# Kernel optimization log

Measured on AMD Instinct MI355X. Metric: run time of the kernel, lower is better.

Reference implementation:

```python
import jax, jax.numpy as jnp
import numpy as np

N = 100000   # nodes
E = 800000   # edges (avg degree 8)
D = 128      # input_dim == output_dim
H = 4        # num_heads
DH = D // H  # head_dim = 32


def setup_inputs() -> dict:
    key = jax.random.key(0)
    ks = jax.random.split(key, 12)
    s = 1.0 / np.sqrt(D)
    x = jax.random.normal(ks[0], (N, D), jnp.float32)
    row = jnp.sort(jax.random.randint(ks[1], (E,), 0, N))  # destination (query) nodes
    col = jax.random.randint(ks[2], (E,), 0, N)            # source (key/value) nodes
    Wq = jax.random.normal(ks[3], (D, D), jnp.float32) * s
    bq = jax.random.normal(ks[4], (D,), jnp.float32) * 0.01
    Wk = jax.random.normal(ks[5], (D, D), jnp.float32) * s
    bk = jax.random.normal(ks[6], (D,), jnp.float32) * 0.01
    Wv = jax.random.normal(ks[7], (D, D), jnp.float32) * s
    bv = jax.random.normal(ks[8], (D,), jnp.float32) * 0.01
    Wo = jax.random.normal(ks[9], (D, D), jnp.float32) * s
    bo = jax.random.normal(ks[10], (D,), jnp.float32) * 0.01
    return {"x": x, "row": row, "col": col, "Wq": Wq, "bq": bq, "Wk": Wk,
            "bk": bk, "Wv": Wv, "bv": bv, "Wo": Wo, "bo": bo}


def reference(x, row, col, Wq, bq, Wk, bk, Wv, bv, Wo, bo):
    n = x.shape[0]
    # projections; reshape (N, head_dim, num_heads) exactly as the torch code
    # NOTE: source scales q by k.size(-1)**0.5 == sqrt(num_heads) (quirk, kept faithful)
    scale = jnp.asarray(H, x.dtype) ** 0.5
    q = ((x @ Wq.T + bq).reshape(n, DH, H)) / scale
    k = (x @ Wk.T + bk).reshape(n, DH, H)
    v = (x @ Wv.T + bv).reshape(n, DH, H)
    # bsddmm: per-edge, per-head scores s[e,h] = q[row[e],:,h] . k[col[e],:,h]
    s = jnp.einsum('edh,edh->eh', q[row], k[col])  # (E, H)
    # sparse row-wise softmax over incoming edges of each destination node
    m = jax.ops.segment_max(s, row, num_segments=n)      # (N, H)
    e = jnp.exp(s - m[row])                               # (E, H)
    z = jax.ops.segment_sum(e, row, num_segments=n)      # (N, H)
    a = e / z[row]                                        # (E, H) attention weights
    # bspmm: y[i,:,h] = sum_{e: row[e]=i} a[e,h] * v[col[e],:,h]
    y = jax.ops.segment_sum(a[:, None, :] * v[col], row, num_segments=n)  # (N, DH, H)
    return y.reshape(n, D) @ Wo.T + bo
```

## Files before the change

### kernel.cpp

```cpp
#include <hip/hip_runtime.h>
#include <hip/hip_bf16.h>
#include <hip/hip_fp16.h>
#include <math.h>

#define D 128
#define H 4

typedef __attribute__((ext_vector_type(8))) short bf16x8;
typedef __attribute__((ext_vector_type(4))) float f32x4;

__device__ __forceinline__ unsigned short f32_to_bf16_rne(float f) {
    union { float f; unsigned u; } c; c.f = f;
    unsigned u = c.u;
    return (unsigned short)((u + 0x7FFFu + ((u >> 16) & 1u)) >> 16);
}
__device__ __forceinline__ float bf16_to_f32(unsigned short h) {
    union { unsigned u; float f; } c; c.u = ((unsigned)h) << 16;
    return c.f;
}

__global__ __launch_bounds__(256) void convert_w(
    const float* __restrict__ Wq, const float* __restrict__ Wk,
    const float* __restrict__ Wv, const float* __restrict__ Wo,
    unsigned short* __restrict__ wh, unsigned short* __restrict__ wl)
{
    int i = blockIdx.x * blockDim.x + threadIdx.x;
    if (i >= D * D) return;
    int r = i >> 7;
    int c = i & 127;
    int pr = ((r & 3) << 5) | (r >> 2);
    int pc = ((c & 3) << 5) | (c >> 2);
    const float* Ws[4] = {Wq, Wk, Wv, Wo};
#pragma unroll
    for (int m = 0; m < 4; ++m) {
        float f = Ws[m][i];
        unsigned short h = f32_to_bf16_rne(f);
        unsigned short l = f32_to_bf16_rne(f - bf16_to_f32(h));
        int dst = (m < 3) ? (pr * D + c) : (r * D + pc);
        wh[m * D * D + dst] = h;
        wl[m * D * D + dst] = l;
    }
}

#define RT 64

template<int NSEL>
__global__ __launch_bounds__(512) void gemm_fused(
    const float* __restrict__ A,
    const unsigned short* __restrict__ whAll, const unsigned short* __restrict__ wlAll,
    const float* __restrict__ b0, const float* __restrict__ b1,
    const float* __restrict__ b2,
    void* __restrict__ o0, void* __restrict__ o1, void* __restrict__ o2,
    float scale0, int n, int wbase, int halfmask, int permBias)
{
    __shared__ unsigned short Ah[RT * 128];
    __shared__ unsigned short Al[RT * 128];

    const int wid  = threadIdx.x >> 6;
    const int lane = threadIdx.x & 63;
    const int quad = lane >> 4;
    const int l16  = lane & 15;
    const int m0   = blockIdx.x * RT;

    for (int idx = threadIdx.x; idx < RT * 16; idx += 512) {
        int r  = idx >> 4;
        int c8 = idx & 15;
        int rg = m0 + r; if (rg > n - 1) rg = n - 1;
        const float4* src = (const float4*)(A + (size_t)rg * D + c8 * 8);
        float4 f0 = src[0], f1 = src[1];
        float fa[8] = {f0.x, f0.y, f0.z, f0.w, f1.x, f1.y, f1.z, f1.w};
        union { bf16x8 v; unsigned short s[8]; } hv, lv;
#pragma unroll
        for (int j = 0; j < 8; ++j) {
            unsigned short hh = f32_to_bf16_rne(fa[j]);
            hv.s[j] = hh;
            lv.s[j] = f32_to_bf16_rne(fa[j] - bf16_to_f32(hh));
        }
        int cs = ((c8 ^ (r & 15)) * 8);
        *(bf16x8*)&Ah[r * 128 + cs] = hv.v;
        *(bf16x8*)&Al[r * 128 + cs] = lv.v;
    }
    __syncthreads();

#pragma unroll 1
    for (int sel = 0; sel < NSEL; ++sel) {
        const unsigned short* wh = whAll + (size_t)(wbase + sel) * D * D;
        const unsigned short* wl = wlAll + (size_t)(wbase + sel) * D * D;
        const float* bias = (sel == 0) ? b0 : (sel == 1 ? b1 : b2);
        void* out        = (sel == 0) ? o0 : (sel == 1 ? o1 : o2);
        const float scale = (sel == 0) ? scale0 : 1.0f;
        const bool halfOut = (halfmask >> sel) & 1;

        const unsigned short* wrh = wh + (size_t)(wid * 16 + l16) * D + quad * 8;
        const unsigned short* wrl = wl + (size_t)(wid * 16 + l16) * D + quad * 8;
        bf16x8 bh[4], bl[4];
#pragma unroll
        for (int kc = 0; kc < 4; ++kc) {
            bh[kc] = *(const bf16x8*)(wrh + kc * 32);
            bl[kc] = *(const bf16x8*)(wrl + kc * 32);
        }

        f32x4 acc[4];
#pragma unroll
        for (int rt = 0; rt < 4; ++rt) acc[rt] = (f32x4){0.f, 0.f, 0.f, 0.f};

#pragma unroll
        for (int kc = 0; kc < 4; ++kc) {
            const int cs = ((quad + 4 * kc) ^ l16) * 8;
            bf16x8 ah[4], al[4];
#pragma unroll
            for (int rt = 0; rt < 4; ++rt) {
                const int r = rt * 16 + l16;
                ah[rt] = *(const bf16x8*)&Ah[r * 128 + cs];
                al[rt] = *(const bf16x8*)&Al[r * 128 + cs];
            }
#pragma unroll
            for (int rt = 0; rt < 4; ++rt)
                acc[rt] = __builtin_amdgcn_mfma_f32_16x16x32_bf16(ah[rt], bh[kc], acc[rt], 0, 0, 0);
#pragma unroll
            for (int rt = 0; rt < 4; ++rt)
                acc[rt] = __builtin_amdgcn_mfma_f32_16x16x32_bf16(al[rt], bh[kc], acc[rt], 0, 0, 0);
#pragma unroll
            for (int rt = 0; rt < 4; ++rt)
                acc[rt] = __builtin_amdgcn_mfma_f32_16x16x32_bf16(ah[rt], bl[kc], acc[rt], 0, 0, 0);
        }

        const int colg = wid * 16 + l16;
        const int bidx = permBias ? (((colg & 31) << 2) | (colg >> 5)) : colg;
        const float bv = bias[bidx];
        if (halfOut) {
            __half* oph = (__half*)out;
#pragma unroll
            for (int rt = 0; rt < 4; ++rt) {
#pragma unroll
                for (int r = 0; r < 4; ++r) {
                    int rowg = m0 + rt * 16 + quad * 4 + r;
                    if (rowg < n)
                        oph[(size_t)rowg * D + colg] = __float2half(acc[rt][r] + bv);
                }
            }
        } else {
            float* opf = (float*)out;
#pragma unroll
            for (int rt = 0; rt < 4; ++rt) {
#pragma unroll
                for (int r = 0; r < 4; ++r) {
                    int rowg = m0 + rt * 16 + quad * 4 + r;
                    if (rowg < n)
                        opf[(size_t)rowg * D + colg] = (acc[rt][r] + bv) * scale;
                }
            }
        }
    }
}

__global__ void build_row_start(const int* __restrict__ row,
                                int* __restrict__ row_start, int n, int e)
{
    int i = blockIdx.x * blockDim.x + threadIdx.x;
    if (i > n) return;
    int lo = 0, hi = e;
    while (lo < hi) {
        int mid = (lo + hi) >> 1;
        if (row[mid] < i) lo = mid + 1; else hi = mid;
    }
    row_start[i] = lo;
}

#define MAXDEG 64
#define WPB 4

template<bool BIG>
__device__ __forceinline__ void edge_loop(
    int lane, int sub, int grp, int deg, int e0,
    const int* cmrow, const int* __restrict__ col,
    const float4 qa, const float4 qb,
    const __half* __restrict__ k, const __half* __restrict__ v,
    float& acc0, float& acc1, float& z)
{
    for (int e = 0; e < deg; e += 4) {
        const int ei = e + grp;
        int c0, c1, c2, c3, cs;
        if (!BIG) {
            const int4 cc = *(const int4*)&cmrow[e];
            c0 = cc.x; c1 = cc.y; c2 = cc.z; c3 = cc.w;
            cs = cmrow[ei < deg ? ei : deg - 1];
        } else {
            int es = ei < deg ? ei : deg - 1;
            cs = col[e0 + es];
            int e1 = e + 1 < deg ? e + 1 : deg - 1;
            int e2 = e + 2 < deg ? e + 2 : deg - 1;
            int e3 = e + 3 < deg ? e + 3 : deg - 1;
            c0 = col[e0 + e];
            c1 = col[e0 + e1];
            c2 = col[e0 + e2];
            c3 = col[e0 + e3];
        }
        __half2 v0 = ((const __half2*)(v + ((size_t)c0 << 7)))[lane];
        __half2 v1 = ((const __half2*)(v + ((size_t)c1 << 7)))[lane];
        __half2 v2 = ((const __half2*)(v + ((size_t)c2 << 7)))[lane];
        __half2 v3 = ((const __half2*)(v + ((size_t)c3 << 7)))[lane];
        union { bf16x8 v8; __half hx[8]; } ku;
        ku.v8 = *(const bf16x8*)(k + ((size_t)cs << 7) + sub * 8);
        float p = qa.x * __half2float(ku.hx[0]) + qa.y * __half2float(ku.hx[1])
                + qa.z * __half2float(ku.hx[2]) + qa.w * __half2float(ku.hx[3])
                + qb.x * __half2float(ku.hx[4]) + qb.y * __half2float(ku.hx[5])
                + qb.z * __half2float(ku.hx[6]) + qb.w * __half2float(ku.hx[7]);
        p += __shfl_xor(p, 1);
        p += __shfl_xor(p, 2);
        float ep = (ei < deg) ? __expf(p) : 0.f;
        float a0 = __shfl(ep,      4 * grp);
        float a1 = __shfl(ep, 16 + 4 * grp);
        float a2 = __shfl(ep, 32 + 4 * grp);
        float a3 = __shfl(ep, 48 + 4 * grp);
        z += (a0 + a1) + (a2 + a3);
        acc0 += a0 * __half2float(v0.x) + a1 * __half2float(v1.x)
              + a2 * __half2float(v2.x) + a3 * __half2float(v3.x);
        acc1 += a0 * __half2float(v0.y) + a1 * __half2float(v1.y)
              + a2 * __half2float(v2.y) + a3 * __half2float(v3.y);
    }
}

__global__ __launch_bounds__(WPB * 64) void edge_attn(
    const int* __restrict__ row_start,
    const float* __restrict__ q, const __half* __restrict__ k,
    const __half* __restrict__ v, const int* __restrict__ col,
    float* __restrict__ y, int n)
{
    __shared__ int cm[WPB][MAXDEG];

    const int wid  = threadIdx.x >> 6;
    const int lane = threadIdx.x & 63;
    const int node = blockIdx.x * WPB + wid;
    if (node >= n) return;

    const int e0  = row_start[node];
    const int deg = row_start[node + 1] - e0;
    const int sub = lane & 15;
    const int grp = lane >> 4;

    const float4* q4 = (const float4*)(q + (size_t)node * D) + sub * 2;
    const float4 qa = q4[0], qb = q4[1];

    float acc0 = 0.f, acc1 = 0.f, z = 0.f;

    if (deg <= MAXDEG) {
        const int dl4 = (deg + 3) & ~3;
        for (int i = lane; i < dl4; i += 64) {
            int ii = i < deg ? i : deg - 1;
            cm[wid][i] = col[e0 + ii];
        }
        edge_loop<false>(lane, sub, grp, deg, e0, cm[wid], col, qa, qb, k, v,
                         acc0, acc1, z);
    } else {
        edge_loop<true>(lane, sub, grp, deg, e0, cm[wid], col, qa, qb, k, v,
                        acc0, acc1, z);
    }

    const float rz = (z > 0.f) ? 1.f / z : 0.f;
    acc0 *= rz;
    acc1 *= rz;

    float2 o; o.x = acc0; o.y = acc1;
    ((float2*)y)[(size_t)node * 64 + lane] = o;
}

extern "C" void kernel_launch(void* const* d_in, const int* in_sizes, int n_in,
                              void* d_out, int out_size, void* d_ws, size_t ws_size,
                              hipStream_t stream)
{
    const float* x   = (const float*)d_in[0];
    const int*   row = (const int*)  d_in[1];
    const int*   col = (const int*)  d_in[2];
    const float* Wq  = (const float*)d_in[3];
    const float* bq  = (const float*)d_in[4];
    const float* Wk  = (const float*)d_in[5];
    const float* bk  = (const float*)d_in[6];
    const float* Wv  = (const float*)d_in[7];
    const float* bv  = (const float*)d_in[8];
    const float* Wo  = (const float*)d_in[9];
    const float* bo  = (const float*)d_in[10];
    float* out = (float*)d_out;

    const int n = in_sizes[0] / D;
    const int e = in_sizes[1];
    const size_t ND = (size_t)n * D;

    float* ws = (float*)d_ws;
    float*  q  = ws;
    __half* kh = (__half*)(ws + ND);
    __half* vh = kh + ND;
    float*  y  = ws + 2 * ND;
    unsigned short* wh = (unsigned short*)(ws + 3 * ND);
    unsigned short* wl = wh + 4 * D * D;
    int* row_start = (int*)(wl + 4 * D * D);

    const int gx = (n + RT - 1) / RT;

    convert_w<<<(D * D + 255) / 256, 256, 0, stream>>>(Wq, Wk, Wv, Wo, wh, wl);

    gemm_fused<3><<<gx, 512, 0, stream>>>(
        x, wh, wl, bq, bk, bv,
        (void*)q, (void*)kh, (void*)vh, 0.5f, n, 0, 6, 1);

    build_row_start<<<(n + 1 + 255) / 256, 256, 0, stream>>>(row, row_start, n, e);

    edge_attn<<<(n + WPB - 1) / WPB, WPB * 64, 0, stream>>>(
        row_start, q, kh, vh, col, y, n);

    gemm_fused<1><<<gx, 512, 0, stream>>>(
        y, wh, wl, bo, bo, bo,
        (void*)out, (void*)out, (void*)out, 1.0f, n, 3, 0, 0);
}
```

Measured before the change: 308.1 us.

## Make projection GEMMs persistent with double-buffered A tiles and per-block weight selection

The fused projection GEMM becomes a persistent kernel with a fixed grid. Each block is assigned one weight matrix, keeps its hi/lo weight fragments in registers, and loops over row tiles. It prefetches the next tile's activations into registers and splits them into a second LDS buffer while the current tile is computed. This aims to hide global-load latency and stop reloading weights per tile. The cost is that each activation tile is now read and split three times (once per Q/K/V block) instead of once, and LDS use doubles, which may reduce occupancy.

Result: faster. 272.8 us (-11.5%).

```diff
diff --git a/kernel.cpp b/kernel.cpp
--- a/kernel.cpp
+++ b/kernel.cpp
@@ -17,6 +17,21 @@
 __device__ __forceinline__ float bf16_to_f32(unsigned short h) {
     union { unsigned u; float f; } c; c.u = ((unsigned)h) << 16;
     return c.f;
+}
+
+__device__ __forceinline__ void split_store(const float4 f0, const float4 f1,
+                                            unsigned short* dh, unsigned short* dl)
+{
+    float fa[8] = {f0.x, f0.y, f0.z, f0.w, f1.x, f1.y, f1.z, f1.w};
+    union { bf16x8 v; unsigned short s[8]; } hv, lv;
+#pragma unroll
+    for (int j = 0; j < 8; ++j) {
+        unsigned short hh = f32_to_bf16_rne(fa[j]);
+        hv.s[j] = hh;
+        lv.s[j] = f32_to_bf16_rne(fa[j] - bf16_to_f32(hh));
+    }
+    *(bf16x8*)dh = hv.v;
+    *(bf16x8*)dl = lv.v;
 }
 
 __global__ __launch_bounds__(256) void convert_w(
@@ -44,60 +59,73 @@
 
 #define RT 64
 
-template<int NSEL>
-__global__ __launch_bounds__(512) void gemm_fused(
+__global__ __launch_bounds__(512) void gemm_pipe(
     const float* __restrict__ A,
     const unsigned short* __restrict__ whAll, const unsigned short* __restrict__ wlAll,
     const float* __restrict__ b0, const float* __restrict__ b1,
     const float* __restrict__ b2,
     void* __restrict__ o0, void* __restrict__ o1, void* __restrict__ o2,
-    float scale0, int n, int wbase, int halfmask, int permBias)
-{
-    __shared__ unsigned short Ah[RT * 128];
-    __shared__ unsigned short Al[RT * 128];
+    float scale0, int n, int wbase, int halfmask, int permBias,
+    int nsel, int gx)
+{
+    __shared__ unsigned short Ah[2][RT * 128];
+    __shared__ unsigned short Al[2][RT * 128];
+
+    const int sel    = blockIdx.x % nsel;
+    const int tile0  = blockIdx.x / nsel;
+    const int tstride = gridDim.x / nsel;
+
+    const unsigned short* wh = whAll + (size_t)(wbase + sel) * D * D;
+    const unsigned short* wl = wlAll + (size_t)(wbase + sel) * D * D;
+    const float* bias = (sel == 0) ? b0 : (sel == 1 ? b1 : b2);
+    void* out        = (sel == 0) ? o0 : (sel == 1 ? o1 : o2);
+    const float scale = (sel == 0) ? scale0 : 1.0f;
+    const bool halfOut = (halfmask >> sel) & 1;
 
     const int wid  = threadIdx.x >> 6;
     const int lane = threadIdx.x & 63;
     const int quad = lane >> 4;
     const int l16  = lane & 15;
-    const int m0   = blockIdx.x * RT;
-
-    for (int idx = threadIdx.x; idx < RT * 16; idx += 512) {
-        int r  = idx >> 4;
-        int c8 = idx & 15;
-        int rg = m0 + r; if (rg > n - 1) rg = n - 1;
-        const float4* src = (const float4*)(A + (size_t)rg * D + c8 * 8);
-        float4 f0 = src[0], f1 = src[1];
-        float fa[8] = {f0.x, f0.y, f0.z, f0.w, f1.x, f1.y, f1.z, f1.w};
-        union { bf16x8 v; unsigned short s[8]; } hv, lv;
-#pragma unroll
-        for (int j = 0; j < 8; ++j) {
-            unsigned short hh = f32_to_bf16_rne(fa[j]);
-            hv.s[j] = hh;
-            lv.s[j] = f32_to_bf16_rne(fa[j] - bf16_to_f32(hh));
-        }
-        int cs = ((c8 ^ (r & 15)) * 8);
-        *(bf16x8*)&Ah[r * 128 + cs] = hv.v;
-        *(bf16x8*)&Al[r * 128 + cs] = lv.v;
+
+    const unsigned short* wrh = wh + (size_t)(wid * 16 + l16) * D + quad * 8;
+    const unsigned short* wrl = wl + (size_t)(wid * 16 + l16) * D + quad * 8;
+    bf16x8 bh[4], bl[4];
+#pragma unroll
+    for (int kc = 0; kc < 4; ++kc) {
+        bh[kc] = *(const bf16x8*)(wrh + kc * 32);
+        bl[kc] = *(const bf16x8*)(wrl + kc * 32);
+    }
+
+    const int idxA = threadIdx.x;
+    const int idxB = threadIdx.x + 512;
+    const int rA = idxA >> 4, cA = idxA & 15;
+    const int rB = idxB >> 4, cB = idxB & 15;
+    const int dA = rA * 128 + ((cA ^ (rA & 15)) * 8);
+    const int dB = rB * 128 + ((cB ^ (rB & 15)) * 8);
+
+    {
+        int rgA = tile0 * RT + rA; if (rgA > n - 1) rgA = n - 1;
+        int rgB = tile0 * RT + rB; if (rgB > n - 1) rgB = n - 1;
+        const float4* pA = (const float4*)(A + (size_t)rgA * D + cA * 8);
+        const float4* pB = (const float4*)(A + (size_t)rgB * D + cB * 8);
+        float4 a0 = pA[0], a1 = pA[1], a2 = pB[0], a3 = pB[1];
+        split_store(a0, a1, &Ah[0][dA], &Al[0][dA]);
+        split_store(a2, a3, &Ah[0][dB], &Al[0][dB]);
     }
     __syncthreads();
 
-#pragma unroll 1
-    for (int sel = 0; sel < NSEL; ++sel) {
-        const unsigned short* wh = whAll + (size_t)(wbase + sel) * D * D;
-        const unsigned short* wl = wlAll + (size_t)(wbase + sel) * D * D;
-        const float* bias = (sel == 0) ? b0 : (sel == 1 ? b1 : b2);
-        void* out        = (sel == 0) ? o0 : (sel == 1 ? o1 : o2);
-        const float scale = (sel == 0) ? scale0 : 1.0f;
-        const bool halfOut = (halfmask >> sel) & 1;
-
-        const unsigned short* wrh = wh + (size_t)(wid * 16 + l16) * D + quad * 8;
-        const unsigned short* wrl = wl + (size_t)(wid * 16 + l16) * D + quad * 8;
-        bf16x8 bh[4], bl[4];
-#pragma unroll
-        for (int kc = 0; kc < 4; ++kc) {
-            bh[kc] = *(const bf16x8*)(wrh + kc * 32);
-            bl[kc] = *(const bf16x8*)(wrl + kc * 32);
+    int cur = 0;
+    for (int t = tile0; t < gx; t += tstride) {
+        const int tn = t + tstride;
+        const bool more = (tn < gx);
+
+        float4 a0, a1, a2, a3;
+        if (more) {
+            int rgA = tn * RT + rA; if (rgA > n - 1) rgA = n - 1;
+            int rgB = tn * RT + rB; if (rgB > n - 1) rgB = n - 1;
+            const float4* pA = (const float4*)(A + (size_t)rgA * D + cA * 8);
+            const float4* pB = (const float4*)(A + (size_t)rgB * D + cB * 8);
+            a0 = pA[0]; a1 = pA[1]; a2 = pB[0]; a3 = pB[1];
         }
 
         f32x4 acc[4];
@@ -111,8 +139,8 @@
 #pragma unroll
             for (int rt = 0; rt < 4; ++rt) {
                 const int r = rt * 16 + l16;
-                ah[rt] = *(const bf16x8*)&Ah[r * 128 + cs];
-                al[rt] = *(const bf16x8*)&Al[r * 128 + cs];
+                ah[rt] = *(const bf16x8*)&Ah[cur][r * 128 + cs];
+                al[rt] = *(const bf16x8*)&Al[cur][r * 128 + cs];
             }
 #pragma unroll
             for (int rt = 0; rt < 4; ++rt)
@@ -125,6 +153,7 @@
                 acc[rt] = __builtin_amdgcn_mfma_f32_16x16x32_bf16(ah[rt], bl[kc], acc[rt], 0, 0, 0);
         }
 
+        const int m0 = t * RT;
         const int colg = wid * 16 + l16;
         const int bidx = permBias ? (((colg & 31) << 2) | (colg >> 5)) : colg;
         const float bv = bias[bidx];
@@ -151,6 +180,13 @@
                 }
             }
         }
+
+        if (more) {
+            split_store(a0, a1, &Ah[cur ^ 1][dA], &Al[cur ^ 1][dA]);
+            split_store(a2, a3, &Ah[cur ^ 1][dB], &Al[cur ^ 1][dB]);
+        }
+        __syncthreads();
+        cur ^= 1;
     }
 }
 
@@ -299,16 +335,18 @@
 
     convert_w<<<(D * D + 255) / 256, 256, 0, stream>>>(Wq, Wk, Wv, Wo, wh, wl);
 
-    gemm_fused<3><<<gx, 512, 0, stream>>>(
+    gemm_pipe<<<768, 512, 0, stream>>>(
         x, wh, wl, bq, bk, bv,
-        (void*)q, (void*)kh, (void*)vh, 0.5f, n, 0, 6, 1);
+        (void*)q, (void*)kh, (void*)vh, 0.5f, n, 0, 6, 1,
+        3, gx);
 
     build_row_start<<<(n + 1 + 255) / 256, 256, 0, stream>>>(row, row_start, n, e);
 
     edge_attn<<<(n + WPB - 1) / WPB, WPB * 64, 0, stream>>>(
         row_start, q, kh, vh, col, y, n);
 
-    gemm_fused<1><<<gx, 512, 0, stream>>>(
+    gemm_pipe<<<512, 512, 0, stream>>>(
         y, wh, wl, bo, bo, bo,
-        (void*)out, (void*)out, (void*)out, 1.0f, n, 3, 0, 0);
-}
+        (void*)out, (void*)out, (void*)out, 1.0f, n, 3, 0, 0,
+        1, gx);
+}
```

## Replace LDS-staged GEMM with direct-register 16-row tiles split across projections

Applied to the files above, without the earlier changes.

Replaces the shared-memory staged 64-row GEMM with a kernel in which each block handles 16 rows, loads and splits the fp32 input into bf16 hi/lo pairs directly in registers, and has each wave compute 32 output columns. The three Q/K/V projections become separate grid-y blocks instead of a serial loop inside one block. This removes the LDS staging and the barrier and raises parallelism. In exchange, each input row is now read and converted three times, once per projection, and the weight fragments are reloaded by many more, smaller blocks.

After: 462.2 us. 50.0% more time.

```diff
diff --git a/kernel.cpp b/kernel.cpp
--- a/kernel.cpp
+++ b/kernel.cpp
@@ -42,10 +42,8 @@
     }
 }
 
-#define RT 64
-
-template<int NSEL>
-__global__ __launch_bounds__(512) void gemm_fused(
+
+__global__ __launch_bounds__(256) void gemm_direct(
     const float* __restrict__ A,
     const unsigned short* __restrict__ whAll, const unsigned short* __restrict__ wlAll,
     const float* __restrict__ b0, const float* __restrict__ b1,
@@ -53,102 +51,79 @@
     void* __restrict__ o0, void* __restrict__ o1, void* __restrict__ o2,
     float scale0, int n, int wbase, int halfmask, int permBias)
 {
-    __shared__ unsigned short Ah[RT * 128];
-    __shared__ unsigned short Al[RT * 128];
+    const int sel = blockIdx.y;
+    const unsigned short* wh = whAll + (size_t)(wbase + sel) * D * D;
+    const unsigned short* wl = wlAll + (size_t)(wbase + sel) * D * D;
+    const float* bias = (sel == 0) ? b0 : (sel == 1 ? b1 : b2);
+    void* out        = (sel == 0) ? o0 : (sel == 1 ? o1 : o2);
+    const float scale = (sel == 0) ? scale0 : 1.0f;
+    const bool halfOut = (halfmask >> sel) & 1;
 
     const int wid  = threadIdx.x >> 6;
     const int lane = threadIdx.x & 63;
     const int quad = lane >> 4;
     const int l16  = lane & 15;
-    const int m0   = blockIdx.x * RT;
-
-    for (int idx = threadIdx.x; idx < RT * 16; idx += 512) {
-        int r  = idx >> 4;
-        int c8 = idx & 15;
-        int rg = m0 + r; if (rg > n - 1) rg = n - 1;
-        const float4* src = (const float4*)(A + (size_t)rg * D + c8 * 8);
-        float4 f0 = src[0], f1 = src[1];
+    const int m0   = blockIdx.x * 16;
+
+    bf16x8 bh[2][4], bl[2][4];
+#pragma unroll
+    for (int s = 0; s < 2; ++s) {
+        const unsigned short* wrh = wh + (size_t)(wid * 32 + s * 16 + l16) * D + quad * 8;
+        const unsigned short* wrl = wl + (size_t)(wid * 32 + s * 16 + l16) * D + quad * 8;
+#pragma unroll
+        for (int kc = 0; kc < 4; ++kc) {
+            bh[s][kc] = *(const bf16x8*)(wrh + kc * 32);
+            bl[s][kc] = *(const bf16x8*)(wrl + kc * 32);
+        }
+    }
+
+    int rga = m0 + l16; if (rga > n - 1) rga = n - 1;
+    const float* ap = A + (size_t)rga * D + quad * 8;
+
+    f32x4 acc0 = (f32x4){0.f, 0.f, 0.f, 0.f};
+    f32x4 acc1 = (f32x4){0.f, 0.f, 0.f, 0.f};
+
+#pragma unroll
+    for (int kc = 0; kc < 4; ++kc) {
+        const float4 f0 = *(const float4*)(ap + kc * 32);
+        const float4 f1 = *(const float4*)(ap + kc * 32 + 4);
         float fa[8] = {f0.x, f0.y, f0.z, f0.w, f1.x, f1.y, f1.z, f1.w};
-        union { bf16x8 v; unsigned short s[8]; } hv, lv;
+        union { bf16x8 v; unsigned short s[8]; } ah, al;
 #pragma unroll
         for (int j = 0; j < 8; ++j) {
             unsigned short hh = f32_to_bf16_rne(fa[j]);
-            hv.s[j] = hh;
-            lv.s[j] = f32_to_bf16_rne(fa[j] - bf16_to_f32(hh));
-        }
-        int cs = ((c8 ^ (r & 15)) * 8);
-        *(bf16x8*)&Ah[r * 128 + cs] = hv.v;
-        *(bf16x8*)&Al[r * 128 + cs] = lv.v;
-    }
-    __syncthreads();
-
-#pragma unroll 1
-    for (int sel = 0; sel < NSEL; ++sel) {
-        const unsigned short* wh = whAll + (size_t)(wbase + sel) * D * D;
-        const unsigned short* wl = wlAll + (size_t)(wbase + sel) * D * D;
-        const float* bias = (sel == 0) ? b0 : (sel == 1 ? b1 : b2);
-        void* out        = (sel == 0) ? o0 : (sel == 1 ? o1 : o2);
-        const float scale = (sel == 0) ? scale0 : 1.0f;
-        const bool halfOut = (halfmask >> sel) & 1;
-
-        const unsigned short* wrh = wh + (size_t)(wid * 16 + l16) * D + quad * 8;
-        const unsigned short* wrl = wl + (size_t)(wid * 16 + l16) * D + quad * 8;
-        bf16x8 bh[4], bl[4];
-#pragma unroll
-        for (int kc = 0; kc < 4; ++kc) {
-            bh[kc] = *(const bf16x8*)(wrh + kc * 32);
-            bl[kc] = *(const bf16x8*)(wrl + kc * 32);
-        }
-
-        f32x4 acc[4];
-#pragma unroll
-        for (int rt = 0; rt < 4; ++rt) acc[rt] = (f32x4){0.f, 0.f, 0.f, 0.f};
-
-#pragma unroll
-        for (int kc = 0; kc < 4; ++kc) {
-            const int cs = ((quad + 4 * kc) ^ l16) * 8;
-            bf16x8 ah[4], al[4];
-#pragma unroll
-            for (int rt = 0; rt < 4; ++rt) {
-                const int r = rt * 16 + l16;
-                ah[rt] = *(const bf16x8*)&Ah[r * 128 + cs];
-                al[rt] = *(const bf16x8*)&Al[r * 128 + cs];
-            }
-#pragma unroll
-            for (int rt = 0; rt < 4; ++rt)
-                acc[rt] = __builtin_amdgcn_mfma_f32_16x16x32_bf16(ah[rt], bh[kc], acc[rt], 0, 0, 0);
-#pragma unroll
-            for (int rt = 0; rt < 4; ++rt)
-                acc[rt] = __builtin_amdgcn_mfma_f32_16x16x32_bf16(al[rt], bh[kc], acc[rt], 0, 0, 0);
-#pragma unroll
-            for (int rt = 0; rt < 4; ++rt)
-                acc[rt] = __builtin_amdgcn_mfma_f32_16x16x32_bf16(ah[rt], bl[kc], acc[rt], 0, 0, 0);
-        }
-
-        const int colg = wid * 16 + l16;
+            ah.s[j] = hh;
+            al.s[j] = f32_to_bf16_rne(fa[j] - bf16_to_f32(hh));
+        }
+        acc0 = __builtin_amdgcn_mfma_f32_16x16x32_bf16(ah.v, bh[0][kc], acc0, 0, 0, 0);
+        acc1 = __builtin_amdgcn_mfma_f32_16x16x32_bf16(ah.v, bh[1][kc], acc1, 0, 0, 0);
+        acc0 = __builtin_amdgcn_mfma_f32_16x16x32_bf16(al.v, bh[0][kc], acc0, 0, 0, 0);
+        acc1 = __builtin_amdgcn_mfma_f32_16x16x32_bf16(al.v, bh[1][kc], acc1, 0, 0, 0);
+        acc0 = __builtin_amdgcn_mfma_f32_16x16x32_bf16(ah.v, bl[0][kc], acc0, 0, 0, 0);
+        acc1 = __builtin_amdgcn_mfma_f32_16x16x32_bf16(ah.v, bl[1][kc], acc1, 0, 0, 0);
+    }
+
+#pragma unroll
+    for (int s = 0; s < 2; ++s) {
+        const f32x4 a = s ? acc1 : acc0;
+        const int colg = wid * 32 + s * 16 + l16;
         const int bidx = permBias ? (((colg & 31) << 2) | (colg >> 5)) : colg;
         const float bv = bias[bidx];
         if (halfOut) {
             __half* oph = (__half*)out;
 #pragma unroll
-            for (int rt = 0; rt < 4; ++rt) {
-#pragma unroll
-                for (int r = 0; r < 4; ++r) {
-                    int rowg = m0 + rt * 16 + quad * 4 + r;
-                    if (rowg < n)
-                        oph[(size_t)rowg * D + colg] = __float2half(acc[rt][r] + bv);
-                }
+            for (int r = 0; r < 4; ++r) {
+                int rowg = m0 + quad * 4 + r;
+                if (rowg < n)
+                    oph[(size_t)rowg * D + colg] = __float2half(a[r] + bv);
             }
         } else {
             float* opf = (float*)out;
 #pragma unroll
-            for (int rt = 0; rt < 4; ++rt) {
-#pragma unroll
-                for (int r = 0; r < 4; ++r) {
-                    int rowg = m0 + rt * 16 + quad * 4 + r;
-                    if (rowg < n)
-                        opf[(size_t)rowg * D + colg] = (acc[rt][r] + bv) * scale;
-                }
+            for (int r = 0; r < 4; ++r) {
+                int rowg = m0 + quad * 4 + r;
+                if (rowg < n)
+                    opf[(size_t)rowg * D + colg] = (a[r] + bv) * scale;
             }
         }
     }
@@ -295,11 +270,11 @@
     unsigned short* wl = wh + 4 * D * D;
     int* row_start = (int*)(wl + 4 * D * D);
 
-    const int gx = (n + RT - 1) / RT;
+    const int ntiles = (n + 15) / 16;
 
     convert_w<<<(D * D + 255) / 256, 256, 0, stream>>>(Wq, Wk, Wv, Wo, wh, wl);
 
-    gemm_fused<3><<<gx, 512, 0, stream>>>(
+    gemm_direct<<<dim3(ntiles, 3), 256, 0, stream>>>(
         x, wh, wl, bq, bk, bv,
         (void*)q, (void*)kh, (void*)vh, 0.5f, n, 0, 6, 1);
 
@@ -308,7 +283,7 @@
     edge_attn<<<(n + WPB - 1) / WPB, WPB * 64, 0, stream>>>(
         row_start, q, kh, vh, col, y, n);
 
-    gemm_fused<1><<<gx, 512, 0, stream>>>(
+    gemm_direct<<<dim3(ntiles, 1), 256, 0, stream>>>(
         y, wh, wl, bo, bo, bo,
         (void*)out, (void*)out, (void*)out, 1.0f, n, 3, 0, 0);
 }
```
